# Kernel tuning notes

Hardware: AMD Instinct MI355X
Metric: run time of the kernel (lower is better)

Reference implementation:

```python
import jax, jax.numpy as jnp
import numpy as np

E, T, D, I = 8, 1024, 2048, 4096  # experts, tokens/expert, model_dim, inner_dim


def setup_inputs() -> dict:
    key = jax.random.key(0)
    k1, k2, k3, k4 = jax.random.split(key, 4)
    scale = 0.02  # keep activations in a sane range
    x = jax.random.normal(k1, (E, T, D), dtype=jnp.float32)
    gate_proj = jax.random.normal(k2, (E * D, I), dtype=jnp.float32) * scale
    inner_proj = jax.random.normal(k3, (E * D, I), dtype=jnp.float32) * scale
    output_proj = jax.random.normal(k4, (E * I, D), dtype=jnp.float32) * scale
    return {"x": x, "gate_proj": gate_proj, "inner_proj": inner_proj,
            "output_proj": output_proj}


def reference(x, gate_proj, inner_proj, output_proj):
    # Fold expert dim out of the weights (matches torch .view in the module).
    gp = gate_proj.reshape(E, D, I)    # (E, D, I)
    ip = inner_proj.reshape(E, D, I)   # (E, D, I)
    op = output_proj.reshape(E, I, D)  # (E, I, D)
    # GLU: silu(x @ gate) * (x @ inner), then project back to model dim.
    g = jnp.einsum('etd,edi->eti', x, gp)        # batched GEMM 1
    h = jax.nn.silu(g) * jnp.einsum('etd,edi->eti', x, ip)  # batched GEMM 2 + gate
    out = jnp.einsum('eti,eid->etd', h, op)      # batched GEMM 3
    return out
```

## Files before the change

### kernel.cpp

```cpp
#include <hip/hip_runtime.h>
#include <cstdint>
#include <cstdio>

typedef unsigned short u16;
typedef unsigned int u32;
typedef __attribute__((ext_vector_type(8))) short short8;
typedef __attribute__((ext_vector_type(4))) float f32x4;

#define E_N 8
#define T_N 1024
#define D_N 2048
#define I_N 4096

__device__ __forceinline__ u16 f2bf(float f) {
  u32 u = __builtin_bit_cast(u32, f);
  u32 r = (u + 0x7FFFu + ((u >> 16) & 1u)) >> 16;
  return (u16)r;
}

__device__ __forceinline__ void g2l16(const void* g, void* l) {
  __builtin_amdgcn_global_load_lds(
      (const __attribute__((address_space(1))) void*)g,
      (__attribute__((address_space(3))) void*)l, 16, 0, 0);
}

__global__ void cvt_x_kernel(const float4* __restrict__ in, uint2* __restrict__ out, int n4) {
  int i = blockIdx.x * blockDim.x + threadIdx.x;
  if (i >= n4) return;
  float4 v = in[i];
  uint2 p;
  p.x = (u32)f2bf(v.x) | ((u32)f2bf(v.y) << 16);
  p.y = (u32)f2bf(v.z) | ((u32)f2bf(v.w) << 16);
  out[i] = p;
}

__global__ void tr_cvt_kernel(const float* __restrict__ in, u16* __restrict__ out,
                              int R, int C) {
  __shared__ u16 tile[64][66];
  int e = blockIdx.z;
  const float* ine = in + (size_t)e * R * C;
  u16* oute = out + (size_t)e * R * C;
  int c0 = blockIdx.x * 64, r0 = blockIdx.y * 64;
  int tid = threadIdx.x;
  int tx = tid & 63, ty = tid >> 6;
#pragma unroll
  for (int rr = ty; rr < 64; rr += 4)
    tile[tx][rr] = f2bf(ine[(size_t)(r0 + rr) * C + c0 + tx]);
  __syncthreads();
  int tx2 = tid & 31, ty2 = tid >> 5;
#pragma unroll
  for (int cc = ty2; cc < 64; cc += 8) {
    u32 v = *(const u32*)&tile[cc][2 * tx2];
    *(u32*)&oute[(size_t)(c0 + cc) * R + r0 + 2 * tx2] = v;
  }
}


#define G3_PHASE(BUF, KH, RH, DOB, STAGE_STMT, GATE_STMT)                                 \
  do {                                                                                    \
    {                                                                                     \
      const u16* ap_ = (const u16*)As + aoff + (BUF) * 16384 + (KH) * 8192 + (RH) * 2048; \
      _Pragma("unroll") for (int mi_ = 0; mi_ < 4; ++mi_)                                 \
          a[mi_] = *(const short8*)(ap_ + mi_ * 512);                                     \
      if (DOB) {                                                                          \
        const u16* bp_ = (const u16*)Bs + boff + (BUF) * 16384 + (KH) * 8192;             \
        _Pragma("unroll") for (int ni_ = 0; ni_ < 4; ++ni_)                               \
            b[ni_] = *(const short8*)(bp_ + ni_ * 512);                                   \
      }                                                                                   \
    }                                                                                     \
    STAGE_STMT;                                                                           \
    __builtin_amdgcn_s_barrier();                                                         \
    asm volatile("s_waitcnt lgkmcnt(0)" ::: "memory");                                    \
    __builtin_amdgcn_sched_barrier(0);                                                    \
    __builtin_amdgcn_s_setprio(1);                                                        \
    _Pragma("unroll") for (int mi_ = 0; mi_ < 4; ++mi_)                                   \
      _Pragma("unroll") for (int ni_ = 0; ni_ < 4; ++ni_)                                 \
        acc[(RH) * 4 + mi_][ni_] = __builtin_amdgcn_mfma_f32_16x16x32_bf16(               \
            a[mi_], b[ni_], acc[(RH) * 4 + mi_][ni_], 0, 0, 0);                           \
    __builtin_amdgcn_s_setprio(0);                                                        \
    GATE_STMT;                                                                            \
    __builtin_amdgcn_s_barrier();                                                         \
  } while (0)

#define G12_PHASE(BUF, KH, RH, DOB, STAGE_STMT, GATE_STMT)                                \
  do {                                                                                    \
    {                                                                                     \
      const u16* ap_ = (const u16*)As + aoff + (BUF) * 16384 + (KH) * 8192 + (RH) * 2048; \
      _Pragma("unroll") for (int mi_ = 0; mi_ < 4; ++mi_)                                 \
          a[mi_] = *(const short8*)(ap_ + mi_ * 512);                                     \
      if (DOB) {                                                                          \
        const u16* bgp_ = (const u16*)Bg + boff + (BUF) * 8192 + (KH) * 4096;             \
        const u16* bip_ = (const u16*)Bi + boff + (BUF) * 8192 + (KH) * 4096;             \
        _Pragma("unroll") for (int ni_ = 0; ni_ < 2; ++ni_) {                             \
          bg[ni_] = *(const short8*)(bgp_ + ni_ * 512);                                   \
          bi[ni_] = *(const short8*)(bip_ + ni_ * 512);                                   \
        }                                                                                 \
      }                                                                                   \
    }                                                                                     \
    STAGE_STMT;                                                                           \
    __builtin_amdgcn_s_barrier();                                                         \
    asm volatile("s_waitcnt lgkmcnt(0)" ::: "memory");                                    \
    __builtin_amdgcn_sched_barrier(0);                                                    \
    __builtin_amdgcn_s_setprio(1);                                                        \
    _Pragma("unroll") for (int mi_ = 0; mi_ < 4; ++mi_)                                   \
      _Pragma("unroll") for (int ni_ = 0; ni_ < 2; ++ni_) {                               \
        accg[(RH) * 4 + mi_][ni_] = __builtin_amdgcn_mfma_f32_16x16x32_bf16(              \
            a[mi_], bg[ni_], accg[(RH) * 4 + mi_][ni_], 0, 0, 0);                         \
        acci[(RH) * 4 + mi_][ni_] = __builtin_amdgcn_mfma_f32_16x16x32_bf16(              \
            a[mi_], bi[ni_], acci[(RH) * 4 + mi_][ni_], 0, 0, 0);                         \
      }                                                                                   \
    __builtin_amdgcn_s_setprio(0);                                                        \
    GATE_STMT;                                                                            \
    __builtin_amdgcn_s_barrier();                                                         \
  } while (0)

__global__ __launch_bounds__(512, 2) void gemm12_kernel(
    const u16* __restrict__ xb, const u16* __restrict__ gT,
    const u16* __restrict__ iT, u16* __restrict__ hb) {
  __shared__ __align__(16) u16 As[32768];
  __shared__ __align__(16) u16 Bg[16384];
  __shared__ __align__(16) u16 Bi[16384];

  const int TM = T_N / 256;
  const int TN = I_N / 128;
  const int PER_E = TM * TN;
  const int NWG = E_N * PER_E;

  int b0 = blockIdx.x;
  int wg = (b0 & 7) * (NWG / 8) + (b0 >> 3);
  int e = wg / PER_E;
  int r = wg % PER_E;
  int tn = r >> 2;
  int tm = r & 3;

  const u16* ae = xb + ((size_t)e * T_N + (size_t)tm * 256) * D_N;
  const u16* ge = gT + ((size_t)e * I_N + (size_t)tn * 128) * D_N;
  const u16* ie = iT + ((size_t)e * I_N + (size_t)tn * 128) * D_N;

  int tid = threadIdx.x;
  int lane = tid & 63, wid = tid >> 6;
  int wm = wid >> 2, wn = wid & 3;
  int fr = lane & 15, quad = lane >> 4;

  int srow = tid >> 2;
  int sg = ((tid & 3) ^ ((srow >> 1) & 3)) * 8;
  int csw = (quad ^ ((fr >> 1) & 3)) * 8;

  int aoff = (wm * 128 + fr) * 32 + csw;
  int boff = (wn * 32 + fr) * 32 + csw;

  auto stageA = [&](int kt, int ks) {
    size_t gk = (size_t)kt * 64 + ks * 32 + sg;
    char* lb = (char*)As + (size_t)((kt & 1) * 2 + ks) * 16384 + wid * 1024;
#pragma unroll
    for (int c = 0; c < 2; ++c)
      g2l16(ae + (size_t)(c * 128 + srow) * D_N + gk, lb + c * 8192);
  };
  auto stageBp = [&](int kt, int ks) {
    size_t go = (size_t)srow * D_N + (size_t)kt * 64 + ks * 32 + sg;
    size_t lo = (size_t)((kt & 1) * 2 + ks) * 8192 + wid * 1024;
    g2l16(ge + go, (char*)Bg + lo);
    g2l16(ie + go, (char*)Bi + lo);
  };

  f32x4 accg[8][2], acci[8][2];
#pragma unroll
  for (int i = 0; i < 8; ++i)
#pragma unroll
    for (int j = 0; j < 2; ++j) {
      accg[i][j] = {0.f, 0.f, 0.f, 0.f};
      acci[i][j] = {0.f, 0.f, 0.f, 0.f};
    }
  short8 a[4], bg[2], bi[2];

  stageA(0, 0); stageBp(0, 0); stageA(0, 1); stageBp(0, 1);
  asm volatile("s_waitcnt vmcnt(4)" ::: "memory");
  __builtin_amdgcn_s_barrier();

  const int NT = D_N / 64;
  for (int t = 0; t < NT; ++t) {
    int buf = t & 1;
    bool pf = (t + 1 < NT);
    G12_PHASE(buf, 0, 0, 1, if (pf) stageA(t + 1, 0), {});
    G12_PHASE(buf, 0, 1, 0, if (pf) stageBp(t + 1, 0),
              if (pf) { asm volatile("s_waitcnt vmcnt(4)" ::: "memory"); }
              else    { asm volatile("s_waitcnt vmcnt(0)" ::: "memory"); });
    G12_PHASE(buf, 1, 0, 1, if (pf) stageA(t + 1, 1), {});
    G12_PHASE(buf, 1, 1, 0, if (pf) stageBp(t + 1, 1),
              if (pf) { asm volatile("s_waitcnt vmcnt(4)" ::: "memory"); });
  }

  u16* he = hb + (size_t)e * T_N * I_N;
  int orow0 = tm * 256 + wm * 128 + quad * 4;
  int ocol0 = tn * 128 + wn * 32 + fr;
#pragma unroll
  for (int mi = 0; mi < 8; ++mi)
#pragma unroll
    for (int ni = 0; ni < 2; ++ni)
#pragma unroll
      for (int rg = 0; rg < 4; ++rg) {
        float g = accg[mi][ni][rg];
        float u = acci[mi][ni][rg];
        float s = g / (1.0f + __expf(-g));
        he[(size_t)(orow0 + mi * 16 + rg) * I_N + ocol0 + ni * 16] = f2bf(s * u);
      }
}

__global__ __launch_bounds__(512, 2) void gemm3_kernel(
    const u16* __restrict__ hb, const u16* __restrict__ oT, float* __restrict__ out) {
  __shared__ __align__(16) u16 As[32768];
  __shared__ __align__(16) u16 Bs[32768];

  const int TM = T_N / 256;
  const int TN = D_N / 256;
  const int PER_E = TM * TN;
  const int NWG = E_N * PER_E;

  int b0 = blockIdx.x;
  int wg = (b0 & 7) * (NWG / 8) + (b0 >> 3);
  int e = wg / PER_E;
  int r = wg % PER_E;
  int tn = r >> 2;
  int tm = r & 3;

  const u16* ae = hb + ((size_t)e * T_N + (size_t)tm * 256) * I_N;
  const u16* be = oT + ((size_t)e * D_N + (size_t)tn * 256) * I_N;

  int tid = threadIdx.x;
  int lane = tid & 63, wid = tid >> 6;
  int wm = wid >> 2, wn = wid & 3;
  int fr = lane & 15, quad = lane >> 4;

  int srow = tid >> 2;
  int sg = ((tid & 3) ^ ((srow >> 1) & 3)) * 8;
  int csw = (quad ^ ((fr >> 1) & 3)) * 8;

  int aoff = (wm * 128 + fr) * 32 + csw;
  int boff = (wn * 64 + fr) * 32 + csw;

  auto stageA = [&](int kt, int ks) {
    size_t gk = (size_t)kt * 64 + ks * 32 + sg;
    char* lb = (char*)As + (size_t)((kt & 1) * 2 + ks) * 16384 + wid * 1024;
#pragma unroll
    for (int c = 0; c < 2; ++c)
      g2l16(ae + (size_t)(c * 128 + srow) * I_N + gk, lb + c * 8192);
  };
  auto stageB = [&](int kt, int ks) {
    size_t gk = (size_t)kt * 64 + ks * 32 + sg;
    char* lb = (char*)Bs + (size_t)((kt & 1) * 2 + ks) * 16384 + wid * 1024;
#pragma unroll
    for (int c = 0; c < 2; ++c)
      g2l16(be + (size_t)(c * 128 + srow) * I_N + gk, lb + c * 8192);
  };

  f32x4 acc[8][4];
#pragma unroll
  for (int i = 0; i < 8; ++i)
#pragma unroll
    for (int j = 0; j < 4; ++j) acc[i][j] = {0.f, 0.f, 0.f, 0.f};
  short8 a[4], b[4];

  stageA(0, 0); stageB(0, 0); stageA(0, 1); stageB(0, 1);
  asm volatile("s_waitcnt vmcnt(4)" ::: "memory");
  __builtin_amdgcn_s_barrier();

  const int NT = I_N / 64;
  for (int t = 0; t < NT; ++t) {
    int buf = t & 1;
    bool pf = (t + 1 < NT);
    G3_PHASE(buf, 0, 0, 1, if (pf) stageA(t + 1, 0), {});
    G3_PHASE(buf, 0, 1, 0, if (pf) stageB(t + 1, 0),
             if (pf) { asm volatile("s_waitcnt vmcnt(4)" ::: "memory"); }
             else    { asm volatile("s_waitcnt vmcnt(0)" ::: "memory"); });
    G3_PHASE(buf, 1, 0, 1, if (pf) stageA(t + 1, 1), {});
    G3_PHASE(buf, 1, 1, 0, if (pf) stageB(t + 1, 1),
             if (pf) { asm volatile("s_waitcnt vmcnt(4)" ::: "memory"); });
  }

  float* oe = out + (size_t)e * T_N * D_N;
  int orow0 = tm * 256 + wm * 128 + quad * 4;
  int ocol0 = tn * 256 + wn * 64 + fr;
#pragma unroll
  for (int mi = 0; mi < 8; ++mi)
#pragma unroll
    for (int ni = 0; ni < 4; ++ni)
#pragma unroll
      for (int rg = 0; rg < 4; ++rg)
        oe[(size_t)(orow0 + mi * 16 + rg) * D_N + ocol0 + ni * 16] = acc[mi][ni][rg];
}

extern "C" void kernel_launch(void* const* d_in, const int* in_sizes, int n_in,
                              void* d_out, int out_size, void* d_ws, size_t ws_size,
                              hipStream_t stream) {
  const float* x = (const float*)d_in[0];
  const float* gp = (const float*)d_in[1];
  const float* ip = (const float*)d_in[2];
  const float* op = (const float*)d_in[3];
  float* out = (float*)d_out;

  const size_t szX = (size_t)E_N * T_N * D_N * 2;
  const size_t szW = (size_t)E_N * D_N * I_N * 2;
  const size_t szH = (size_t)E_N * T_N * I_N * 2;
  const size_t need = szX + 3 * szW + szH;
  if (ws_size < need) {
    fprintf(stderr, "kernel_launch: ws_size %zu < needed %zu\n", ws_size, need);
    return;
  }

  char* w = (char*)d_ws;
  u16* xb = (u16*)w; w += szX;
  u16* gT = (u16*)w; w += szW;
  u16* iT = (u16*)w; w += szW;
  u16* oTt = (u16*)w; w += szW;
  u16* hb = (u16*)w; w += szH;

  int n4 = E_N * T_N * D_N / 4;
  cvt_x_kernel<<<(n4 + 255) / 256, 256, 0, stream>>>((const float4*)x, (uint2*)xb, n4);
  dim3 tg1(I_N / 64, D_N / 64, E_N);
  tr_cvt_kernel<<<tg1, 256, 0, stream>>>(gp, gT, D_N, I_N);
  tr_cvt_kernel<<<tg1, 256, 0, stream>>>(ip, iT, D_N, I_N);
  dim3 tg2(D_N / 64, I_N / 64, E_N);
  tr_cvt_kernel<<<tg2, 256, 0, stream>>>(op, oTt, I_N, D_N);

  gemm12_kernel<<<E_N * (T_N / 256) * (I_N / 128), 512, 0, stream>>>(xb, gT, iT, hb);
  gemm3_kernel<<<E_N * (T_N / 256) * (D_N / 256), 512, 0, stream>>>(hb, oTt, out);
}
```

Before: 1.255 ms.

## Deepen GEMM LDS pipeline to four k-slots with prefetch distance three

Both GEMM kernels move from a double-buffered 64-wide k-tile loop to a four-slot ring of 32-wide k-steps, issuing async global-to-LDS loads three steps ahead with graded vmcnt waits. The aim is to hide global memory latency behind more in-flight loads. The transpose-convert kernel also switches to float4 loads and 8-byte stores with a wider padded tile. The deeper pipeline issues more barriers per unit of k-work, and the new LDS padding may introduce bank conflicts.

```diff
diff --git a/kernel.cpp b/kernel.cpp
--- a/kernel.cpp
+++ b/kernel.cpp
@@ -36,82 +36,86 @@
 
 __global__ void tr_cvt_kernel(const float* __restrict__ in, u16* __restrict__ out,
                               int R, int C) {
-  __shared__ u16 tile[64][66];
+  __shared__ u16 tile[64][72];
   int e = blockIdx.z;
   const float* ine = in + (size_t)e * R * C;
   u16* oute = out + (size_t)e * R * C;
   int c0 = blockIdx.x * 64, r0 = blockIdx.y * 64;
   int tid = threadIdx.x;
-  int tx = tid & 63, ty = tid >> 6;
-#pragma unroll
-  for (int rr = ty; rr < 64; rr += 4)
-    tile[tx][rr] = f2bf(ine[(size_t)(r0 + rr) * C + c0 + tx]);
+  int tx = tid & 15, ty = tid >> 4;
+#pragma unroll
+  for (int rr = ty; rr < 64; rr += 16) {
+    float4 v = *(const float4*)&ine[(size_t)(r0 + rr) * C + c0 + tx * 4];
+    tile[tx * 4 + 0][rr] = f2bf(v.x);
+    tile[tx * 4 + 1][rr] = f2bf(v.y);
+    tile[tx * 4 + 2][rr] = f2bf(v.z);
+    tile[tx * 4 + 3][rr] = f2bf(v.w);
+  }
   __syncthreads();
-  int tx2 = tid & 31, ty2 = tid >> 5;
-#pragma unroll
-  for (int cc = ty2; cc < 64; cc += 8) {
-    u32 v = *(const u32*)&tile[cc][2 * tx2];
-    *(u32*)&oute[(size_t)(c0 + cc) * R + r0 + 2 * tx2] = v;
-  }
-}
-
-
-#define G3_PHASE(BUF, KH, RH, DOB, STAGE_STMT, GATE_STMT)                                 \
-  do {                                                                                    \
-    {                                                                                     \
-      const u16* ap_ = (const u16*)As + aoff + (BUF) * 16384 + (KH) * 8192 + (RH) * 2048; \
-      _Pragma("unroll") for (int mi_ = 0; mi_ < 4; ++mi_)                                 \
-          a[mi_] = *(const short8*)(ap_ + mi_ * 512);                                     \
-      if (DOB) {                                                                          \
-        const u16* bp_ = (const u16*)Bs + boff + (BUF) * 16384 + (KH) * 8192;             \
-        _Pragma("unroll") for (int ni_ = 0; ni_ < 4; ++ni_)                               \
-            b[ni_] = *(const short8*)(bp_ + ni_ * 512);                                   \
-      }                                                                                   \
-    }                                                                                     \
-    STAGE_STMT;                                                                           \
-    __builtin_amdgcn_s_barrier();                                                         \
-    asm volatile("s_waitcnt lgkmcnt(0)" ::: "memory");                                    \
-    __builtin_amdgcn_sched_barrier(0);                                                    \
-    __builtin_amdgcn_s_setprio(1);                                                        \
-    _Pragma("unroll") for (int mi_ = 0; mi_ < 4; ++mi_)                                   \
-      _Pragma("unroll") for (int ni_ = 0; ni_ < 4; ++ni_)                                 \
-        acc[(RH) * 4 + mi_][ni_] = __builtin_amdgcn_mfma_f32_16x16x32_bf16(               \
-            a[mi_], b[ni_], acc[(RH) * 4 + mi_][ni_], 0, 0, 0);                           \
-    __builtin_amdgcn_s_setprio(0);                                                        \
-    GATE_STMT;                                                                            \
-    __builtin_amdgcn_s_barrier();                                                         \
+#pragma unroll
+  for (int cc = ty; cc < 64; cc += 16) {
+    uint2 v = *(const uint2*)&tile[cc][tx * 4];
+    *(uint2*)&oute[(size_t)(c0 + cc) * R + r0 + tx * 4] = v;
+  }
+}
+
+
+#define G3_PHASE(SLOT, RH, DOB, STAGE_STMT, GATE_STMT)                                 \
+  do {                                                                                 \
+    {                                                                                  \
+      const u16* ap_ = (const u16*)As + aoff + (SLOT) * 8192 + (RH) * 2048;            \
+      _Pragma("unroll") for (int mi_ = 0; mi_ < 4; ++mi_)                              \
+          a[mi_] = *(const short8*)(ap_ + mi_ * 512);                                  \
+      if (DOB) {                                                                       \
+        const u16* bp_ = (const u16*)Bs + boff + (SLOT) * 8192;                        \
+        _Pragma("unroll") for (int ni_ = 0; ni_ < 4; ++ni_)                            \
+            b[ni_] = *(const short8*)(bp_ + ni_ * 512);                                \
+      }                                                                                \
+    }                                                                                  \
+    STAGE_STMT;                                                                        \
+    __builtin_amdgcn_s_barrier();                                                      \
+    asm volatile("s_waitcnt lgkmcnt(0)" ::: "memory");                                 \
+    __builtin_amdgcn_sched_barrier(0);                                                 \
+    __builtin_amdgcn_s_setprio(1);                                                     \
+    _Pragma("unroll") for (int mi_ = 0; mi_ < 4; ++mi_)                                \
+      _Pragma("unroll") for (int ni_ = 0; ni_ < 4; ++ni_)                              \
+        acc[(RH) * 4 + mi_][ni_] = __builtin_amdgcn_mfma_f32_16x16x32_bf16(            \
+            a[mi_], b[ni_], acc[(RH) * 4 + mi_][ni_], 0, 0, 0);                        \
+    __builtin_amdgcn_s_setprio(0);                                                     \
+    GATE_STMT;                                                                         \
+    __builtin_amdgcn_s_barrier();                                                      \
   } while (0)
 
-#define G12_PHASE(BUF, KH, RH, DOB, STAGE_STMT, GATE_STMT)                                \
-  do {                                                                                    \
-    {                                                                                     \
-      const u16* ap_ = (const u16*)As + aoff + (BUF) * 16384 + (KH) * 8192 + (RH) * 2048; \
-      _Pragma("unroll") for (int mi_ = 0; mi_ < 4; ++mi_)                                 \
-          a[mi_] = *(const short8*)(ap_ + mi_ * 512);                                     \
-      if (DOB) {                                                                          \
-        const u16* bgp_ = (const u16*)Bg + boff + (BUF) * 8192 + (KH) * 4096;             \
-        const u16* bip_ = (const u16*)Bi + boff + (BUF) * 8192 + (KH) * 4096;             \
-        _Pragma("unroll") for (int ni_ = 0; ni_ < 2; ++ni_) {                             \
-          bg[ni_] = *(const short8*)(bgp_ + ni_ * 512);                                   \
-          bi[ni_] = *(const short8*)(bip_ + ni_ * 512);                                   \
-        }                                                                                 \
-      }                                                                                   \
-    }                                                                                     \
-    STAGE_STMT;                                                                           \
-    __builtin_amdgcn_s_barrier();                                                         \
-    asm volatile("s_waitcnt lgkmcnt(0)" ::: "memory");                                    \
-    __builtin_amdgcn_sched_barrier(0);                                                    \
-    __builtin_amdgcn_s_setprio(1);                                                        \
-    _Pragma("unroll") for (int mi_ = 0; mi_ < 4; ++mi_)                                   \
-      _Pragma("unroll") for (int ni_ = 0; ni_ < 2; ++ni_) {                               \
-        accg[(RH) * 4 + mi_][ni_] = __builtin_amdgcn_mfma_f32_16x16x32_bf16(              \
-            a[mi_], bg[ni_], accg[(RH) * 4 + mi_][ni_], 0, 0, 0);                         \
-        acci[(RH) * 4 + mi_][ni_] = __builtin_amdgcn_mfma_f32_16x16x32_bf16(              \
-            a[mi_], bi[ni_], acci[(RH) * 4 + mi_][ni_], 0, 0, 0);                         \
-      }                                                                                   \
-    __builtin_amdgcn_s_setprio(0);                                                        \
-    GATE_STMT;                                                                            \
-    __builtin_amdgcn_s_barrier();                                                         \
+#define G12_PHASE(SLOT, RH, DOB, STAGE_STMT, GATE_STMT)                                \
+  do {                                                                                 \
+    {                                                                                  \
+      const u16* ap_ = (const u16*)As + aoff + (SLOT) * 8192 + (RH) * 2048;            \
+      _Pragma("unroll") for (int mi_ = 0; mi_ < 4; ++mi_)                              \
+          a[mi_] = *(const short8*)(ap_ + mi_ * 512);                                  \
+      if (DOB) {                                                                       \
+        const u16* bgp_ = (const u16*)Bg + boff + (SLOT) * 4096;                       \
+        const u16* bip_ = (const u16*)Bi + boff + (SLOT) * 4096;                       \
+        _Pragma("unroll") for (int ni_ = 0; ni_ < 2; ++ni_) {                          \
+          bg[ni_] = *(const short8*)(bgp_ + ni_ * 512);                                \
+          bi[ni_] = *(const short8*)(bip_ + ni_ * 512);                                \
+        }                                                                              \
+      }                                                                                \
+    }                                                                                  \
+    STAGE_STMT;                                                                        \
+    __builtin_amdgcn_s_barrier();                                                      \
+    asm volatile("s_waitcnt lgkmcnt(0)" ::: "memory");                                 \
+    __builtin_amdgcn_sched_barrier(0);                                                 \
+    __builtin_amdgcn_s_setprio(1);                                                     \
+    _Pragma("unroll") for (int mi_ = 0; mi_ < 4; ++mi_)                                \
+      _Pragma("unroll") for (int ni_ = 0; ni_ < 2; ++ni_) {                            \
+        accg[(RH) * 4 + mi_][ni_] = __builtin_amdgcn_mfma_f32_16x16x32_bf16(           \
+            a[mi_], bg[ni_], accg[(RH) * 4 + mi_][ni_], 0, 0, 0);                      \
+        acci[(RH) * 4 + mi_][ni_] = __builtin_amdgcn_mfma_f32_16x16x32_bf16(           \
+            a[mi_], bi[ni_], acci[(RH) * 4 + mi_][ni_], 0, 0, 0);                      \
+      }                                                                                \
+    __builtin_amdgcn_s_setprio(0);                                                     \
+    GATE_STMT;                                                                         \
+    __builtin_amdgcn_s_barrier();                                                      \
   } while (0)
 
 __global__ __launch_bounds__(512, 2) void gemm12_kernel(
@@ -149,16 +153,16 @@
   int aoff = (wm * 128 + fr) * 32 + csw;
   int boff = (wn * 32 + fr) * 32 + csw;
 
-  auto stageA = [&](int kt, int ks) {
-    size_t gk = (size_t)kt * 64 + ks * 32 + sg;
-    char* lb = (char*)As + (size_t)((kt & 1) * 2 + ks) * 16384 + wid * 1024;
+  auto stageA = [&](int s) {
+    size_t gk = (size_t)s * 32 + sg;
+    char* lb = (char*)As + (size_t)(s & 3) * 16384 + wid * 1024;
 #pragma unroll
     for (int c = 0; c < 2; ++c)
       g2l16(ae + (size_t)(c * 128 + srow) * D_N + gk, lb + c * 8192);
   };
-  auto stageBp = [&](int kt, int ks) {
-    size_t go = (size_t)srow * D_N + (size_t)kt * 64 + ks * 32 + sg;
-    size_t lo = (size_t)((kt & 1) * 2 + ks) * 8192 + wid * 1024;
+  auto stageBp = [&](int s) {
+    size_t go = (size_t)srow * D_N + (size_t)s * 32 + sg;
+    size_t lo = (size_t)(s & 3) * 8192 + wid * 1024;
     g2l16(ge + go, (char*)Bg + lo);
     g2l16(ie + go, (char*)Bi + lo);
   };
@@ -173,21 +177,19 @@
     }
   short8 a[4], bg[2], bi[2];
 
-  stageA(0, 0); stageBp(0, 0); stageA(0, 1); stageBp(0, 1);
-  asm volatile("s_waitcnt vmcnt(4)" ::: "memory");
+  stageA(0); stageBp(0); stageA(1); stageBp(1); stageA(2); stageBp(2);
+  asm volatile("s_waitcnt vmcnt(8)" ::: "memory");
   __builtin_amdgcn_s_barrier();
 
-  const int NT = D_N / 64;
-  for (int t = 0; t < NT; ++t) {
-    int buf = t & 1;
-    bool pf = (t + 1 < NT);
-    G12_PHASE(buf, 0, 0, 1, if (pf) stageA(t + 1, 0), {});
-    G12_PHASE(buf, 0, 1, 0, if (pf) stageBp(t + 1, 0),
-              if (pf) { asm volatile("s_waitcnt vmcnt(4)" ::: "memory"); }
-              else    { asm volatile("s_waitcnt vmcnt(0)" ::: "memory"); });
-    G12_PHASE(buf, 1, 0, 1, if (pf) stageA(t + 1, 1), {});
-    G12_PHASE(buf, 1, 1, 0, if (pf) stageBp(t + 1, 1),
-              if (pf) { asm volatile("s_waitcnt vmcnt(4)" ::: "memory"); });
+  const int NS = D_N / 32;
+  for (int s = 0; s < NS; ++s) {
+    int slot = s & 3;
+    bool pf = (s + 3 < NS);
+    G12_PHASE(slot, 0, 1, if (pf) stageA(s + 3), {});
+    G12_PHASE(slot, 1, 0, if (pf) stageBp(s + 3),
+              if (s + 3 < NS)      { asm volatile("s_waitcnt vmcnt(8)" ::: "memory"); }
+              else if (s + 2 < NS) { asm volatile("s_waitcnt vmcnt(4)" ::: "memory"); }
+              else if (s + 1 < NS) { asm volatile("s_waitcnt vmcnt(0)" ::: "memory"); });
   }
 
   u16* he = hb + (size_t)e * T_N * I_N;
@@ -238,16 +240,16 @@
   int aoff = (wm * 128 + fr) * 32 + csw;
   int boff = (wn * 64 + fr) * 32 + csw;
 
-  auto stageA = [&](int kt, int ks) {
-    size_t gk = (size_t)kt * 64 + ks * 32 + sg;
-    char* lb = (char*)As + (size_t)((kt & 1) * 2 + ks) * 16384 + wid * 1024;
+  auto stageA = [&](int s) {
+    size_t gk = (size_t)s * 32 + sg;
+    char* lb = (char*)As + (size_t)(s & 3) * 16384 + wid * 1024;
 #pragma unroll
     for (int c = 0; c < 2; ++c)
       g2l16(ae + (size_t)(c * 128 + srow) * I_N + gk, lb + c * 8192);
   };
-  auto stageB = [&](int kt, int ks) {
-    size_t gk = (size_t)kt * 64 + ks * 32 + sg;
-    char* lb = (char*)Bs + (size_t)((kt & 1) * 2 + ks) * 16384 + wid * 1024;
+  auto stageB = [&](int s) {
+    size_t gk = (size_t)s * 32 + sg;
+    char* lb = (char*)Bs + (size_t)(s & 3) * 16384 + wid * 1024;
 #pragma unroll
     for (int c = 0; c < 2; ++c)
       g2l16(be + (size_t)(c * 128 + srow) * I_N + gk, lb + c * 8192);
@@ -260,21 +262,19 @@
     for (int j = 0; j < 4; ++j) acc[i][j] = {0.f, 0.f, 0.f, 0.f};
   short8 a[4], b[4];
 
-  stageA(0, 0); stageB(0, 0); stageA(0, 1); stageB(0, 1);
-  asm volatile("s_waitcnt vmcnt(4)" ::: "memory");
+  stageA(0); stageB(0); stageA(1); stageB(1); stageA(2); stageB(2);
+  asm volatile("s_waitcnt vmcnt(8)" ::: "memory");
   __builtin_amdgcn_s_barrier();
 
-  const int NT = I_N / 64;
-  for (int t = 0; t < NT; ++t) {
-    int buf = t & 1;
-    bool pf = (t + 1 < NT);
-    G3_PHASE(buf, 0, 0, 1, if (pf) stageA(t + 1, 0), {});
-    G3_PHASE(buf, 0, 1, 0, if (pf) stageB(t + 1, 0),
-             if (pf) { asm volatile("s_waitcnt vmcnt(4)" ::: "memory"); }
-             else    { asm volatile("s_waitcnt vmcnt(0)" ::: "memory"); });
-    G3_PHASE(buf, 1, 0, 1, if (pf) stageA(t + 1, 1), {});
-    G3_PHASE(buf, 1, 1, 0, if (pf) stageB(t + 1, 1),
-             if (pf) { asm volatile("s_waitcnt vmcnt(4)" ::: "memory"); });
+  const int NS = I_N / 32;
+  for (int s = 0; s < NS; ++s) {
+    int slot = s & 3;
+    bool pf = (s + 3 < NS);
+    G3_PHASE(slot, 0, 1, if (pf) stageA(s + 3), {});
+    G3_PHASE(slot, 1, 0, if (pf) stageB(s + 3),
+             if (s + 3 < NS)      { asm volatile("s_waitcnt vmcnt(8)" ::: "memory"); }
+             else if (s + 2 < NS) { asm volatile("s_waitcnt vmcnt(4)" ::: "memory"); }
+             else if (s + 1 < NS) { asm volatile("s_waitcnt vmcnt(0)" ::: "memory"); });
   }
 
   float* oe = out + (size_t)e * T_N * D_N;
```

After: 1.221 ms. -2.7%, faster.
